# Kernel tuning notes

Hardware: AMD Instinct MI355X
Metric: run time of the kernel (lower is better)

Reference implementation:

```python
import jax, jax.numpy as jnp
import numpy as np

B, K, N, T, C = 2, 2, 4096, 8, 3
H = 192            # hidden_dim
NODE_DIM = 10
N_LAYERS = 10
KNN = 16           # k nearest neighbours
TOP_FRAC = 0.4
SHARP = 5.0        # mask_sharpness
S = max(int(TOP_FRAC * N), KNN + 1)   # n_select per graph


def _ln(x, g, b, eps=1e-5):
    mu = x.mean(-1, keepdims=True)
    v = ((x - mu) ** 2).mean(-1, keepdims=True)  # biased var, matches nn.LayerNorm
    return (x - mu) / jnp.sqrt(v + eps) * g + b


def setup_inputs() -> dict:
    key = jax.random.key(0)
    ks = jax.random.split(key, 12)
    rn = lambda k, shape: 0.05 * jax.random.normal(k, shape, jnp.float32)
    F0 = 2 * NODE_DIM + 4   # first EdgeConv MLP in-dim
    FR = 2 * H + 4          # remaining EdgeConv MLP in-dim
    L = N_LAYERS - 1
    return {
        "u_base": jax.random.normal(ks[0], (B, K, N, C), jnp.float32),
        "pos": jax.random.uniform(ks[1], (B, N, 3), dtype=jnp.float32),
        "velocity_in": jax.random.normal(ks[2], (B, T, N, C), jnp.float32),
        "airfoil_mask": (jax.random.uniform(ks[3], (B, N)) < 0.05).astype(jnp.float32),
        "conv0_w1": rn(ks[4], (F0, H)), "conv0_b1": jnp.zeros((H,)),
        "conv0_w2": rn(ks[5], (H, H)), "conv0_b2": jnp.zeros((H,)),
        "conv0_g": jnp.ones((H,)), "conv0_be": jnp.zeros((H,)),
        "convs_w1": rn(ks[6], (L, FR, H)), "convs_b1": jnp.zeros((L, H)),
        "convs_w2": rn(ks[7], (L, H, H)), "convs_b2": jnp.zeros((L, H)),
        "convs_g": jnp.ones((L, H)), "convs_be": jnp.zeros((L, H)),
        "head_g": jnp.ones((H,)), "head_be": jnp.zeros((H,)),
        "head_w1": rn(ks[8], (H, H)), "head_b1": jnp.zeros((H,)),
        "head_w2": rn(ks[9], (H, 3)), "head_b2": jnp.zeros((3,)),
    }


def reference(u_base, pos, velocity_in, airfoil_mask,
              conv0_w1, conv0_b1, conv0_w2, conv0_b2, conv0_g, conv0_be,
              convs_w1, convs_b1, convs_w2, convs_b2, convs_g, convs_be,
              head_g, head_be, head_w1, head_b1, head_w2, head_b2):
    # --- variance gating (torch .var/.std are unbiased) ---
    var_pp = jnp.var(velocity_in, axis=1, ddof=1).sum(-1)                      # [B,N]
    var_z = (var_pp - var_pp.mean(1, keepdims=True)) / (
        jnp.std(var_pp, axis=1, ddof=1, keepdims=True) + 1e-8)
    soft_mask = jax.nn.sigmoid(SHARP * var_z) * (1.0 - airfoil_mask)           # [B,N]

    # --- select top-variance points per graph ---
    _, top_idx = jax.lax.top_k(var_pp, S)                                      # [B,S]
    pos_sel = jnp.take_along_axis(pos, top_idx[..., None], axis=1)             # [B,S,3]
    mask_sel = jnp.take_along_axis(soft_mask, top_idx, axis=1)[..., None]      # [B,S,1]
    v_last = velocity_in[:, -1]                                                # [B,N,C]
    ub_sel = jnp.take_along_axis(u_base, top_idx[:, None, :, None], axis=2)    # [B,K,S,C]
    vl_sel = jnp.take_along_axis(v_last, top_idx[..., None], axis=1)           # [B,S,C]
    vf_sel = jnp.take_along_axis(var_pp[..., None], top_idx[..., None], axis=1)
    static = jnp.concatenate([vl_sel, pos_sel, vf_sel], -1)                    # [B,S,7]
    x0 = jnp.concatenate(
        [ub_sel, jnp.broadcast_to(static[:, None], (B, K, S, 7))], -1)         # [B,K,S,10]

    def per_graph(x, pos_b):  # x: [K,S,F0], pos_b: [S,3]
        # kNN graph (self excluded via +inf diagonal, as in the chunked cdist)
        d2 = jnp.sum((pos_b[:, None] - pos_b[None]) ** 2, -1)                  # [S,S]
        d2 = d2.at[jnp.arange(S), jnp.arange(S)].set(jnp.inf)
        _, knn = jax.lax.top_k(-d2, KNN)                                       # [S,KNN]
        # PyG convention with edge_index=stack([targets, sources]):
        # i = edge_index[1] = knn neighbours, j = edge_index[0] = centre nodes
        idx_i = knn.reshape(-1)                     # [E] aggregation targets
        idx_j = jnp.repeat(jnp.arange(S), KNN)      # [E]
        rel = pos_b[idx_i] - pos_b[idx_j]           # pos[edge_index[1]] - pos[edge_index[0]]
        dist = jnp.linalg.norm(rel, axis=-1, keepdims=True)
        ea = jnp.concatenate([rel, dist], -1)       # [E,4]
        ea_b = jnp.broadcast_to(ea, (K,) + ea.shape)

        def conv(h, w1, b1, w2, b2, g, be):
            hi = h[:, idx_i]
            hj = h[:, idx_j]
            m = jnp.concatenate([hi, hj - hi, ea_b], -1)                       # [K,E,2F+4]
            m = jax.nn.gelu(m @ w1 + b1, approximate=False) @ w2 + b2          # [K,E,H]
            agg = jnp.zeros((K, S, H), h.dtype).at[:, idx_i].add(m)
            return _ln(agg, g, be)

        h = conv(x, conv0_w1, conv0_b1, conv0_w2, conv0_b2, conv0_g, conv0_be)
        for l in range(N_LAYERS - 1):
            h = conv(h, convs_w1[l], convs_b1[l], convs_w2[l], convs_b2[l],
                     convs_g[l], convs_be[l]) + h
        hh = _ln(h, head_g, head_be)
        return jax.nn.gelu(hh @ head_w1 + head_b1, approximate=False) @ head_w2 + head_b2

    delta = jax.vmap(per_graph)(x0, pos_sel)        # [B,K,S,3]
    delta = delta * mask_sel[:, None]               # [B,1,S,1]

    def scatter_b(idx, d):  # idx [S], d [K,S,3]
        return jnp.zeros((K, N, C), d.dtype).at[:, idx].set(d)

    delta_full = jax.vmap(scatter_b)(top_idx, delta)            # [B,K,N,C]
    return (u_base + delta_full) * (1.0 - airfoil_mask)[:, None, :, None]
```

## Files before the change

### kernel.cpp

```cpp
#include <hip/hip_runtime.h>
#include <hip/hip_bf16.h>
#include <math.h>

#define B_ 2
#define K_ 2
#define NN_ 4096
#define T_ 8
#define C_ 3
#define H_ 192
#define S_ 1638
#define KK_ 16
#define E_ (S_*KK_)
#define NROW (B_*K_*S_)
#define SHARP_ 5.0f

typedef __hip_bfloat16 bf;
typedef unsigned long long ull;
typedef __bf16 bf16x8 __attribute__((ext_vector_type(8)));
typedef float f32x4 __attribute__((ext_vector_type(4)));

__device__ int   g_isbf16;
__device__ __align__(16) float g_var[B_*NN_];
__device__ __align__(16) float g_vs1[B_*16];
__device__ __align__(16) float g_vs2[B_*16];
__device__ __align__(16) int   g_topidx[B_*S_];
__device__ __align__(16) float g_possel[B_*S_*3];
__device__ __align__(16) float g_masksel[B_*S_];
__device__ __align__(16) float g_x0[NROW*10];
__device__ __align__(16) int   g_knn[B_*E_];
__device__ __align__(16) float g_ea[B_*E_*4];
__device__ __align__(16) int   g_indeg[B_*S_];
__device__ __align__(16) int   g_cursor[B_*S_];
__device__ __align__(16) int   g_off[B_*(S_+1)];
__device__ __align__(16) int   g_list[B_*E_];
__device__ __align__(16) float g_P[(size_t)NROW*H_];
__device__ __align__(16) bf    g_Qbf[(size_t)NROW*H_];
__device__ __align__(16) float g_h[(size_t)NROW*H_];
__device__ __align__(16) bf    g_w2p[(size_t)11*H_*H_];
__device__ __align__(16) bf    g_wcp[(size_t)9*H_*384];

__device__ __forceinline__ float bf2f(bf x){ return __bfloat162float(x); }
__device__ __forceinline__ float LD(const void* p, long i){
  return g_isbf16 ? __bfloat162float(((const bf*)p)[i]) : ((const float*)p)[i];
}
__device__ __forceinline__ float LDi(const void* p, long i, int isb){
  return isb ? __bfloat162float(((const bf*)p)[i]) : ((const float*)p)[i];
}
__device__ __forceinline__ float gelu_f(float x){ return 0.5f*x*(1.0f + erff(x*0.70710678118654752f)); }
__device__ __forceinline__ ull shfl_xor_u64(ull v, int m){
  unsigned lo = (unsigned)v, hi = (unsigned)(v >> 32);
  lo = __shfl_xor(lo, m, 64); hi = __shfl_xor(hi, m, 64);
  return ((ull)hi << 32) | lo;
}

__global__ __launch_bounds__(256) void k_var(const void* __restrict__ vel,
                                             const void* __restrict__ ub,
                                             const void* __restrict__ pos){
  __shared__ int s_bad;
  int b = blockIdx.y;
  int bx = blockIdx.x;
  int tid = threadIdx.x;
  if (tid == 0) s_bad = 0;
  __syncthreads();
  {
    const bf* pa = (const bf*)ub; const bf* pb = (const bf*)pos; const bf* pc = (const bf*)vel;
    int bad = 0;
    #pragma unroll
    for (int s = 0; s < 2; ++s){
      float va = __bfloat162float(pa[tid + s*256]);
      float vb = __bfloat162float(pb[tid + s*256]);
      float vc = __bfloat162float(pc[tid + s*256]);
      if (!(fabsf(va) <= 1000.f)) bad = 1;
      if (!(fabsf(vb) <= 1000.f)) bad = 1;
      if (!(fabsf(vc) <= 1000.f)) bad = 1;
    }
    if (bad) atomicOr(&s_bad, 1);
  }
  __syncthreads();
  int isb = (s_bad == 0) ? 1 : 0;
  if (bx == 0 && b == 0 && tid == 0) g_isbf16 = isb;
  int zi = (b*16 + bx)*256 + tid;
  if (zi < B_*S_){ g_indeg[zi] = 0; g_cursor[zi] = 0; }
  int n = bx*256 + tid;
  float v = 0.f;
  #pragma unroll
  for (int c = 0; c < 3; ++c){
    float x[8];
    #pragma unroll
    for (int t = 0; t < 8; ++t)
      x[t] = LDi(vel, ((long)(b*T_+t)*NN_ + n)*3 + c, isb);
    float m = __fadd_rn(__fadd_rn(__fadd_rn(x[0],x[1]), __fadd_rn(x[2],x[3])),
                        __fadd_rn(__fadd_rn(x[4],x[5]), __fadd_rn(x[6],x[7]))) / 8.0f;
    float d[8];
    #pragma unroll
    for (int t = 0; t < 8; ++t){ float dd = __fadd_rn(x[t], -m); d[t] = __fmul_rn(dd,dd); }
    float sv = __fadd_rn(__fadd_rn(__fadd_rn(d[0],d[1]), __fadd_rn(d[2],d[3])),
                         __fadd_rn(__fadd_rn(d[4],d[5]), __fadd_rn(d[6],d[7])));
    v = __fadd_rn(v, sv / 7.0f);
  }
  g_var[b*NN_ + n] = v;
  float s1 = v, s2 = v*v;
  #pragma unroll
  for (int o = 32; o; o >>= 1){ s1 += __shfl_xor(s1,o,64); s2 += __shfl_xor(s2,o,64); }
  __shared__ float r1[4], r2[4];
  int lane = tid & 63, wid = tid >> 6;
  if (!lane){ r1[wid]=s1; r2[wid]=s2; }
  __syncthreads();
  if (tid == 0){
    g_vs1[b*16 + bx] = r1[0]+r1[1]+r1[2]+r1[3];
    g_vs2[b*16 + bx] = r2[0]+r2[1]+r2[2]+r2[3];
  }
}

__global__ __launch_bounds__(256) void k_rank(){
  int b = blockIdx.y;
  int i = blockIdx.x*4 + (threadIdx.x >> 6);
  int lane = threadIdx.x & 63;
  float vi = g_var[b*NN_+i];
  int rank = 0;
  for (int j = lane; j < NN_; j += 64){
    float vj = g_var[b*NN_+j];
    rank += ((vj > vi) || (vj == vi && j < i)) ? 1 : 0;
  }
  #pragma unroll
  for (int o = 32; o; o >>= 1) rank += __shfl_xor(rank, o, 64);
  if (lane == 0 && rank < S_) g_topidx[b*S_ + rank] = i;
}

__global__ void k_gather(const void* __restrict__ pos, const void* __restrict__ ub,
                         const void* __restrict__ vel, const void* __restrict__ air){
  int gi = blockIdx.x*256 + threadIdx.x;
  if (gi >= B_*S_) return;
  int b = gi / S_, s = gi - b*S_;
  int node = g_topidx[gi];
  float px = LD(pos, ((long)b*NN_+node)*3+0);
  float py = LD(pos, ((long)b*NN_+node)*3+1);
  float pz = LD(pos, ((long)b*NN_+node)*3+2);
  g_possel[gi*3+0]=px; g_possel[gi*3+1]=py; g_possel[gi*3+2]=pz;
  float S1 = 0.f, S2 = 0.f;
  #pragma unroll
  for (int t = 0; t < 16; ++t){ S1 += g_vs1[b*16+t]; S2 += g_vs2[b*16+t]; }
  float mean = S1*(1.f/NN_);
  float sd = sqrtf(fmaxf((S2 - S1*S1*(1.f/NN_))*(1.f/(NN_-1)), 0.f));
  float vf = g_var[b*NN_+node];
  float z = (vf-mean)/(sd+1e-8f);
  float sig = 1.f/(1.f+expf(-SHARP_*z));
  g_masksel[gi] = sig*(1.f - LD(air, b*NN_+node));
  float vl0 = LD(vel, ((long)(b*T_+7)*NN_+node)*3+0);
  float vl1 = LD(vel, ((long)(b*T_+7)*NN_+node)*3+1);
  float vl2 = LD(vel, ((long)(b*T_+7)*NN_+node)*3+2);
  for (int k = 0; k < K_; ++k){
    long row = (long)(b*K_+k)*S_ + s;
    float* x = g_x0 + row*10;
    x[0]=LD(ub, ((long)(b*K_+k)*NN_+node)*3+0);
    x[1]=LD(ub, ((long)(b*K_+k)*NN_+node)*3+1);
    x[2]=LD(ub, ((long)(b*K_+k)*NN_+node)*3+2);
    x[3]=vl0; x[4]=vl1; x[5]=vl2;
    x[6]=px;  x[7]=py;  x[8]=pz;
    x[9]=vf;
  }
}

__global__ __launch_bounds__(256) void k_knn(){
  __shared__ float px[S_], py[S_], pz[S_];
  int b = blockIdx.y;
  int j = blockIdx.x*4 + (threadIdx.x >> 6);
  int lane = threadIdx.x & 63;
  for (int t = threadIdx.x; t < S_; t += 256){
    px[t] = g_possel[(b*S_+t)*3+0];
    py[t] = g_possel[(b*S_+t)*3+1];
    pz[t] = g_possel[(b*S_+t)*3+2];
  }
  __syncthreads();
  if (j >= S_) return;
  float xj=px[j], yj=py[j], zj=pz[j];
  float dist[KK_]; int id[KK_];
  #pragma unroll
  for (int t = 0; t < KK_; ++t){ dist[t]=3.0e38f; id[t]=0x7fffffff; }
  for (int c = lane; c < S_; c += 64){
    if (c == j) continue;
    float dx=__fadd_rn(px[c],-xj), dy=__fadd_rn(py[c],-yj), dz=__fadd_rn(pz[c],-zj);
    float d2 = __fadd_rn(__fadd_rn(__fmul_rn(dx,dx), __fmul_rn(dy,dy)), __fmul_rn(dz,dz));
    if (d2 < dist[KK_-1]){
      int p = 0;
      #pragma unroll
      for (int q = 0; q < KK_; ++q) p += (dist[q] <= d2) ? 1 : 0;
      #pragma unroll
      for (int q = KK_-1; q >= 1; --q){
        bool mv = (q > p);
        dist[q] = mv ? dist[q-1] : dist[q];
        id[q]   = mv ? id[q-1]   : id[q];
      }
      #pragma unroll
      for (int q = 0; q < KK_; ++q){ if (q == p){ dist[q] = d2; id[q] = c; } }
    }
  }
  ull mykey = 0;
  #pragma unroll
  for (int t = 0; t < KK_; ++t){
    ull k = (((ull)__float_as_uint(dist[0])) << 32) | (unsigned)id[0];
    ull m = k;
    #pragma unroll
    for (int o = 32; o; o >>= 1){ ull other = shfl_xor_u64(m, o); m = (other < m) ? other : m; }
    if (k == m){
      #pragma unroll
      for (int q = 0; q < KK_-1; ++q){ dist[q]=dist[q+1]; id[q]=id[q+1]; }
      dist[KK_-1] = 3.0e38f; id[KK_-1] = 0x7fffffff;
    }
    if (lane == t) mykey = m;
  }
  if (lane < KK_){
    int i = (int)(mykey & 0xffffffffu);
    g_knn[(b*S_+j)*KK_ + lane] = i;
    float rx = __fadd_rn(px[i],-xj), ry = __fadd_rn(py[i],-yj), rz = __fadd_rn(pz[i],-zj);
    float dd = sqrtf(__fadd_rn(__fadd_rn(__fmul_rn(rx,rx), __fmul_rn(ry,ry)), __fmul_rn(rz,rz)));
    float* o = g_ea + ((long)b*E_ + j*KK_ + lane)*4;
    o[0]=rx; o[1]=ry; o[2]=rz; o[3]=dd;
    atomicAdd(&g_indeg[b*S_+i], 1);
  }
}

__global__ void k_scan(){
  __shared__ int sA[2048], sB[2048];
  int b = blockIdx.x, tid = threadIdx.x;
  for (int i = tid; i < 2048; i += 1024) sA[i] = (i < S_) ? g_indeg[b*S_+i] : 0;
  __syncthreads();
  int *src = sA, *dst = sB;
  for (int d = 1; d < 2048; d <<= 1){
    for (int i = tid; i < 2048; i += 1024) dst[i] = src[i] + (i >= d ? src[i-d] : 0);
    __syncthreads();
    int* t2 = src; src = dst; dst = t2;
  }
  if (tid == 0) g_off[b*(S_+1)] = 0;
  for (int i = tid; i < S_; i += 1024) g_off[b*(S_+1)+i+1] = src[i];
}

#define PW2_BLKS 1584
#define PWC_BLKS 2592
#define INIT_BLKS 192
#define FILL_BLKS 205
#define PROJ_BLKS 410
__global__ void k_packall(const void* __restrict__ c0w2, const void* __restrict__ cw2,
                          const void* __restrict__ hw1, const void* __restrict__ cw1,
                          const void* __restrict__ ub, const void* __restrict__ air,
                          float* __restrict__ out, const void* __restrict__ c0w1){
  int blk = blockIdx.x;
  if (blk < PW2_BLKS){
    int gi = blk*256 + threadIdx.x;
    if (gi >= 11*H_*H_) return;
    int mat = gi / (H_*H_), r = gi - mat*(H_*H_);
    int k = r / H_, n = r - (r/H_)*H_;
    float v;
    if (mat == 0)      v = LD(c0w2, (long)k*H_ + n);
    else if (mat <= 9) v = LD(cw2, (long)(mat-1)*H_*H_ + (long)k*H_ + n);
    else               v = LD(hw1, (long)k*H_ + n);
    int t = k>>5, q = (k>>3)&3, jj = k&7;
    g_w2p[(size_t)mat*H_*H_ + (((t*4+q)*H_ + n)*8 + jj)] = __float2bfloat16(v);
  } else if (blk < PW2_BLKS + PWC_BLKS){
    int gi = (blk - PW2_BLKS)*256 + threadIdx.x;
    if (gi >= 9*H_*384) return;
    int l = gi / (H_*384), r = gi - l*(H_*384);
    int k = r / 384, n = r - (r/384)*384;
    long base = (long)l*388*H_;
    float v;
    if (n < H_) v = LD(cw1, base + (long)k*H_ + n) - LD(cw1, base + (long)(H_+k)*H_ + n);
    else        v = LD(cw1, base + (long)(H_+k)*H_ + (n-H_));
    int t = k>>5, q = (k>>3)&3, jj = k&7;
    g_wcp[(size_t)l*(H_*384) + (((t*4+q)*384 + n)*8 + jj)] = __float2bfloat16(v);
  } else if (blk < PW2_BLKS + PWC_BLKS + INIT_BLKS){
    int gi = (blk - PW2_BLKS - PWC_BLKS)*256 + threadIdx.x;
    int n = (gi/3) % NN_;
    int b = gi / (K_*NN_*C_);
    float a = 1.f - LD(air, b*NN_+n);
    out[gi] = LD(ub, gi) * a;
  } else if (blk < PW2_BLKS + PWC_BLKS + INIT_BLKS + FILL_BLKS){
    int idx = (blk - PW2_BLKS - PWC_BLKS - INIT_BLKS)*256 + threadIdx.x;
    if (idx >= B_*E_) return;
    int b = idx / E_, e = idx - b*E_;
    int i = g_knn[idx];
    int slot = atomicAdd(&g_cursor[b*S_+i], 1);
    g_list[b*E_ + g_off[b*(S_+1)+i] + slot] = e;
  } else {
    __shared__ float xs[16][10];
    __shared__ float wP[10][192];
    __shared__ float wQ[10][192];
    int tid = threadIdx.x;
    long rowBase = (long)(blk - PW2_BLKS - PWC_BLKS - INIT_BLKS - FILL_BLKS) * 16;
    for (int idx = tid; idx < 1920; idx += 256){
      int f = idx / 192, n = idx - (idx/192)*192;
      float a = LD(c0w1, f*H_+n), b = LD(c0w1, (10+f)*H_+n);
      wP[f][n] = a - b; wQ[f][n] = b;
    }
    for (int idx = tid; idx < 160; idx += 256){
      int r = idx / 10, f = idx - (idx/10)*10;
      long row = rowBase + r; if (row >= NROW) row = NROW-1;
      xs[r][f] = g_x0[row*10 + f];
    }
    __syncthreads();
    for (int o = tid; o < 16*384; o += 256){
      int r = o / 384, n = o - (o/384)*384;
      long row = rowBase + r;
      if (row >= NROW) continue;
      float acc = 0.f;
      if (n < 192){
        #pragma unroll
        for (int f = 0; f < 10; ++f) acc += xs[r][f]*wP[f][n];
        g_P[row*192 + n] = acc;
      } else {
        int nc = n - 192;
        #pragma unroll
        for (int f = 0; f < 10; ++f) acc += xs[r][f]*wQ[f][nc];
        g_Qbf[row*192 + nc] = __float2bfloat16(acc);
      }
    }
  }
}

template<int RES, int DOPQ, int DOHEAD>
__global__ __launch_bounds__(256) void k_layer(
    const void* __restrict__ w1cB, long w1cO,
    const void* __restrict__ b1B, long b1O,
    const void* __restrict__ biasB, long biasO,
    const void* __restrict__ gB, long gO,
    const void* __restrict__ beB, long beO,
    int bOff, int pqOff,
    const void* __restrict__ hg, const void* __restrict__ hbe,
    const void* __restrict__ hb1, const void* __restrict__ hw2,
    const void* __restrict__ hb2, const void* __restrict__ ubase,
    const void* __restrict__ air, float* __restrict__ out,
    int M){
  int wv = threadIdx.x >> 6, lane = threadIdx.x & 63;
  int q = lane >> 4, l16 = lane & 15;
  long rowBase = (long)blockIdx.x * 8;
  __shared__ bf    sbf[16][200];
  __shared__ float tile[8][200];
  __shared__ float ws0[192], ws1[192], ws2[192], ws3[192], b1s[192], gs[192], bes[192];
  __shared__ float srow[8], rrow[8];
  for (int c = threadIdx.x; c < 192; c += 256){
    ws0[c] = LD(w1cB, w1cO+c);
    ws1[c] = LD(w1cB, w1cO+H_+c);
    ws2[c] = LD(w1cB, w1cO+2*H_+c);
    ws3[c] = LD(w1cB, w1cO+3*H_+c);
    b1s[c] = LD(b1B, b1O+c);
    gs[c]  = LD(gB, gO+c);
    bes[c] = LD(beB, beO+c);
  }
  for (int o = threadIdx.x; o < 8*192; o += 256){
    int lr = o / 192, col = o - lr*192;
    sbf[8+lr][col] = __float2bfloat16(0.f);
  }
  __syncthreads();
  for (int rr = 0; rr < 2; ++rr){
    int lrow = wv*2 + rr;
    long row = rowBase + lrow;
    int bk = (int)(row / S_); int i = (int)(row - (long)bk*S_); int b = bk >> 1;
    int off = __builtin_amdgcn_readfirstlane(g_off[b*(S_+1)+i]);
    int deg = __builtin_amdgcn_readfirstlane(g_off[b*(S_+1)+i+1]) - off;
    const int* lst = g_list + b*E_ + off;
    const bf* Q = g_Qbf + (size_t)bk*S_*H_;
    const float* EA = g_ea + (size_t)b*E_*4;
    int c0 = lane, c1 = lane+64, c2 = lane+128;
    float w00=ws0[c0], w01=ws1[c0], w02=ws2[c0], w03=ws3[c0];
    float w10=ws0[c1], w11=ws1[c1], w12=ws2[c1], w13=ws3[c1];
    float w20=ws0[c2], w21=ws1[c2], w22=ws2[c2], w23=ws3[c2];
    float base0 = g_P[(size_t)row*H_+c0] + b1s[c0];
    float base1 = g_P[(size_t)row*H_+c1] + b1s[c1];
    float base2 = g_P[(size_t)row*H_+c2] + b1s[c2];
    float acc0=0.f, acc1=0.f, acc2=0.f;
    int d = 0;
    for (; d + 2 <= deg; d += 2){
      int e0 = __builtin_amdgcn_readfirstlane(lst[d]);
      int e1 = __builtin_amdgcn_readfirstlane(lst[d+1]);
      float4 a0 = *reinterpret_cast<const float4*>(EA + (size_t)e0*4);
      float4 a1 = *reinterpret_cast<const float4*>(EA + (size_t)e1*4);
      const bf* Q0 = Q + (size_t)(e0>>4)*H_;
      const bf* Q1 = Q + (size_t)(e1>>4)*H_;
      float q00=bf2f(Q0[c0]), q01=bf2f(Q0[c1]), q02=bf2f(Q0[c2]);
      float q10=bf2f(Q1[c0]), q11=bf2f(Q1[c1]), q12=bf2f(Q1[c2]);
      float g00 = gelu_f(base0 + q00 + a0.x*w00 + a0.y*w01 + a0.z*w02 + a0.w*w03);
      float g01 = gelu_f(base1 + q01 + a0.x*w10 + a0.y*w11 + a0.z*w12 + a0.w*w13);
      float g02 = gelu_f(base2 + q02 + a0.x*w20 + a0.y*w21 + a0.z*w22 + a0.w*w23);
      float g10 = gelu_f(base0 + q10 + a1.x*w00 + a1.y*w01 + a1.z*w02 + a1.w*w03);
      float g11 = gelu_f(base1 + q11 + a1.x*w10 + a1.y*w11 + a1.z*w12 + a1.w*w13);
      float g12 = gelu_f(base2 + q12 + a1.x*w20 + a1.y*w21 + a1.z*w22 + a1.w*w23);
      acc0 += g00; acc0 += g10;
      acc1 += g01; acc1 += g11;
      acc2 += g02; acc2 += g12;
    }
    for (; d < deg; ++d){
      int e = __builtin_amdgcn_readfirstlane(lst[d]);
      float4 a = *reinterpret_cast<const float4*>(EA + (size_t)e*4);
      const bf* Qe = Q + (size_t)(e>>4)*H_;
      acc0 += gelu_f(base0 + bf2f(Qe[c0]) + a.x*w00 + a.y*w01 + a.z*w02 + a.w*w03);
      acc1 += gelu_f(base1 + bf2f(Qe[c1]) + a.x*w10 + a.y*w11 + a.z*w12 + a.w*w13);
      acc2 += gelu_f(base2 + bf2f(Qe[c2]) + a.x*w20 + a.y*w21 + a.z*w22 + a.w*w23);
    }
    sbf[lrow][c0] = __float2bfloat16(acc0);
    sbf[lrow][c1] = __float2bfloat16(acc1);
    sbf[lrow][c2] = __float2bfloat16(acc2);
  }
  __syncthreads();
  {
    const bf* Bp = g_w2p + bOff;
    f32x4 acc[3];
    #pragma unroll
    for (int ct = 0; ct < 3; ++ct) acc[ct] = (f32x4){0.f,0.f,0.f,0.f};
    #pragma unroll
    for (int t = 0; t < 6; ++t){
      int kof = t*32 + q*8;
      bf16x8 af = *reinterpret_cast<const bf16x8*>(&sbf[l16][kof]);
      #pragma unroll
      for (int ct = 0; ct < 3; ++ct){
        int n = wv*48 + ct*16 + l16;
        bf16x8 bfr = *reinterpret_cast<const bf16x8*>(Bp + (((t*4+q)*192 + n)*8));
        acc[ct] = __builtin_amdgcn_mfma_f32_16x16x32_bf16(af, bfr, acc[ct], 0,0,0);
      }
    }
    float degf[4];
    #pragma unroll
    for (int r = 0; r < 4; ++r){
      int lr = q*4 + r;
      if (lr < 8){
        long row = rowBase + lr;
        int bk = (int)(row / S_); int i = (int)(row - (long)bk*S_); int b = bk >> 1;
        degf[r] = (float)(g_off[b*(S_+1)+i+1] - g_off[b*(S_+1)+i]);
      } else degf[r] = 0.f;
    }
    #pragma unroll
    for (int ct = 0; ct < 3; ++ct){
      int col = wv*48 + ct*16 + l16;
      float bb = LD(biasB, biasO + col);
      #pragma unroll
      for (int r = 0; r < 4; ++r){
        int lr = q*4 + r;
        if (lr < 8) tile[lr][col] = acc[ct][r] + degf[r]*bb;
      }
    }
  }
  __syncthreads();
  {
    int lr = threadIdx.x >> 5;
    int k32 = threadIdx.x & 31;
    float s = 0.f, qq = 0.f;
    #pragma unroll
    for (int c6 = 0; c6 < 6; ++c6){ float x = tile[lr][k32 + c6*32]; s += x; qq += x*x; }
    #pragma unroll
    for (int o = 1; o < 32; o <<= 1){ s += __shfl_xor(s,o,64); qq += __shfl_xor(qq,o,64); }
    if (k32 == 0){
      float mu = s*(1.f/H_);
      float var = qq*(1.f/H_) - mu*mu;
      srow[lr] = mu;
      rrow[lr] = rsqrtf(fmaxf(var, 0.f) + 1e-5f);
    }
  }
  __syncthreads();
  for (int o = threadIdx.x; o < 8*192; o += 256){
    int lr = o / 192, col = o - lr*192;
    long row = rowBase + lr;
    float y = (tile[lr][col] - srow[lr])*rrow[lr]*gs[col] + bes[col];
    if (RES) y += g_h[(size_t)row*192 + col];
    if (!DOHEAD) g_h[(size_t)row*192 + col] = y;
    sbf[lr][col] = __float2bfloat16(y);
    if (DOHEAD) tile[lr][col] = y;
  }
  if (DOPQ){
    __syncthreads();
    const bf* Bq = g_wcp + pqOff;
    f32x4 acc2[6];
    #pragma unroll
    for (int ct = 0; ct < 6; ++ct) acc2[ct] = (f32x4){0.f,0.f,0.f,0.f};
    #pragma unroll
    for (int t = 0; t < 6; ++t){
      int kof = t*32 + q*8;
      bf16x8 af = *reinterpret_cast<const bf16x8*>(&sbf[l16][kof]);
      #pragma unroll
      for (int ct = 0; ct < 6; ++ct){
        int n = wv*96 + ct*16 + l16;
        bf16x8 bfr = *reinterpret_cast<const bf16x8*>(Bq + (((t*4+q)*384 + n)*8));
        acc2[ct] = __builtin_amdgcn_mfma_f32_16x16x32_bf16(af, bfr, acc2[ct], 0,0,0);
      }
    }
    #pragma unroll
    for (int ct = 0; ct < 6; ++ct){
      int col = wv*96 + ct*16 + l16;
      #pragma unroll
      for (int r = 0; r < 4; ++r){
        int orow = q*4 + r;
        if (orow < 8){
          long row = rowBase + orow;
          float v = acc2[ct][r];
          if (col < 192) g_P[(size_t)row*192 + col] = v;
          else           g_Qbf[(size_t)row*192 + (col-192)] = __float2bfloat16(v);
        }
      }
    }
  }
  if (DOHEAD){
    __syncthreads();
    {
      int lr = threadIdx.x >> 5;
      int k32 = threadIdx.x & 31;
      float s = 0.f, qq = 0.f;
      #pragma unroll
      for (int c6 = 0; c6 < 6; ++c6){ float x = tile[lr][k32 + c6*32]; s += x; qq += x*x; }
      #pragma unroll
      for (int o = 1; o < 32; o <<= 1){ s += __shfl_xor(s,o,64); qq += __shfl_xor(qq,o,64); }
      if (k32 == 0){
        float mu = s*(1.f/H_);
        float var = qq*(1.f/H_) - mu*mu;
        srow[lr] = mu;
        rrow[lr] = rsqrtf(fmaxf(var, 0.f) + 1e-5f);
      }
    }
    __syncthreads();
    for (int o = threadIdx.x; o < 8*192; o += 256){
      int lr = o / 192, col = o - lr*192;
      sbf[lr][col] = __float2bfloat16((tile[lr][col] - srow[lr])*rrow[lr]*LD(hg,col) + LD(hbe,col));
    }
    __syncthreads();
    {
      const bf* Bp = g_w2p + 10*H_*H_;
      f32x4 hacc[3];
      #pragma unroll
      for (int ct = 0; ct < 3; ++ct) hacc[ct] = (f32x4){0.f,0.f,0.f,0.f};
      #pragma unroll
      for (int t = 0; t < 6; ++t){
        int kof = t*32 + q*8;
        bf16x8 af = *reinterpret_cast<const bf16x8*>(&sbf[l16][kof]);
        #pragma unroll
        for (int ct = 0; ct < 3; ++ct){
          int n = wv*48 + ct*16 + l16;
          bf16x8 bfr = *reinterpret_cast<const bf16x8*>(Bp + (((t*4+q)*192 + n)*8));
          hacc[ct] = __builtin_amdgcn_mfma_f32_16x16x32_bf16(af, bfr, hacc[ct], 0,0,0);
        }
      }
      #pragma unroll
      for (int ct = 0; ct < 3; ++ct){
        int col = wv*48 + ct*16 + l16;
        float bb = LD(hb1, col);
        #pragma unroll
        for (int r = 0; r < 4; ++r){
          int lr = q*4 + r;
          if (lr < 8) tile[lr][col] = gelu_f(hacc[ct][r] + bb);
        }
      }
    }
    __syncthreads();
    {
      int r = threadIdx.x >> 5, k32 = threadIdx.x & 31;
      float p0 = 0.f, p1 = 0.f, p2 = 0.f;
      #pragma unroll
      for (int c6 = 0; c6 < 6; ++c6){
        int col = k32 + c6*32;
        float tv = tile[r][col];
        p0 += tv*LD(hw2, col*3+0);
        p1 += tv*LD(hw2, col*3+1);
        p2 += tv*LD(hw2, col*3+2);
      }
      #pragma unroll
      for (int o = 1; o < 32; o <<= 1){
        p0 += __shfl_xor(p0,o,64);
        p1 += __shfl_xor(p1,o,64);
        p2 += __shfl_xor(p2,o,64);
      }
      if (k32 == 0){
        long row = rowBase + r;
        int bk = (int)(row / S_), s = (int)(row - (long)bk*S_), b = bk >> 1;
        float msk = g_masksel[b*S_+s];
        int node = g_topidx[b*S_+s];
        float am = 1.f - LD(air, b*NN_+node);
        float d0 = p0 + LD(hb2,0), d1 = p1 + LD(hb2,1), d2 = p2 + LD(hb2,2);
        long oi = ((long)bk*NN_ + node)*3;
        out[oi+0] = (LD(ubase, oi+0) + d0*msk)*am;
        out[oi+1] = (LD(ubase, oi+1) + d1*msk)*am;
        out[oi+2] = (LD(ubase, oi+2) + d2*msk)*am;
      }
    }
  }
}

extern "C" void kernel_launch(void* const* d_in, const int* in_sizes, int n_in,
                              void* d_out, int out_size, void* d_ws, size_t ws_size,
                              hipStream_t stream) {
  (void)in_sizes; (void)n_in; (void)d_ws; (void)ws_size; (void)out_size;
  const void* u_base = d_in[0];
  const void* pos    = d_in[1];
  const void* vel    = d_in[2];
  const void* air    = d_in[3];
  const void* c0w1   = d_in[4];
  const void* c0b1   = d_in[5];
  const void* c0w2   = d_in[6];
  const void* c0b2   = d_in[7];
  const void* c0g    = d_in[8];
  const void* c0be   = d_in[9];
  const void* cw1    = d_in[10];
  const void* cb1    = d_in[11];
  const void* cw2    = d_in[12];
  const void* cb2    = d_in[13];
  const void* cg     = d_in[14];
  const void* cbe    = d_in[15];
  const void* hg     = d_in[16];
  const void* hbe    = d_in[17];
  const void* hw1    = d_in[18];
  const void* hb1    = d_in[19];
  const void* hw2    = d_in[20];
  const void* hb2    = d_in[21];
  float* out = (float*)d_out;

  k_var<<<dim3(16, B_), 256, 0, stream>>>(vel, u_base, pos);
  k_rank<<<dim3(NN_/4, B_), 256, 0, stream>>>();
  k_gather<<<13, 256, 0, stream>>>(pos, u_base, vel, air);
  k_knn<<<dim3((S_+3)/4, B_), 256, 0, stream>>>();
  k_scan<<<B_, 1024, 0, stream>>>();
  k_packall<<<PW2_BLKS + PWC_BLKS + INIT_BLKS + FILL_BLKS + PROJ_BLKS, 256, 0, stream>>>(
      c0w2, cw2, hw1, cw1, u_base, air, out, c0w1);

  const int GN8 = NROW / 8;
  for (int l = 0; l < 10; ++l){
    long w1cO = (l == 0) ? 20L*H_ : ((long)(l-1)*388 + 384)*H_;
    const void* w1cB = (l == 0) ? c0w1 : cw1;
    long lOff = (l == 0) ? 0 : (long)(l-1)*H_;
    const void* b1B = (l == 0) ? c0b1 : cb1;
    const void* b2B = (l == 0) ? c0b2 : cb2;
    const void* gB  = (l == 0) ? c0g  : cg;
    const void* beB = (l == 0) ? c0be : cbe;
    if (l == 0)
      k_layer<0,1,0><<<GN8, 256, 0, stream>>>(w1cB, w1cO, b1B, lOff, b2B, lOff, gB, lOff, beB, lOff,
                                              0, 0, hg, hbe, hb1, hw2, hb2, u_base, air, out, NROW);
    else if (l < 9)
      k_layer<1,1,0><<<GN8, 256, 0, stream>>>(w1cB, w1cO, b1B, lOff, b2B, lOff, gB, lOff, beB, lOff,
                                              l*H_*H_, l*H_*384, hg, hbe, hb1, hw2, hb2, u_base, air, out, NROW);
    else
      k_layer<1,0,1><<<GN8, 256, 0, stream>>>(w1cB, w1cO, b1B, lOff, b2B, lOff, gB, lOff, beB, lOff,
                                              l*H_*H_, 0, hg, hbe, hb1, hw2, hb2, u_base, air, out, NROW);
  }
}
```

Measured before the change: 667.0 us.

## Use 512-thread layer blocks with one row per wave and ping-pong Q buffers

The per-layer kernel now runs with 512 threads, so each of the 8 waves handles one destination row instead of two. The MFMA column tiles, the LayerNorm reductions and the head reductions are remapped to match. The edge gather loop is unrolled by 4 instead of 2, exposing more independent loads and GELU evaluations per wave. The Q projection is double-buffered by layer parity, so a layer no longer overwrites Q values that other blocks may still be reading. This adds extra global memory and leaves some waves idle in the 192-column GEMM, since only 12 tiles are spread over 8 waves.

```diff
diff --git a/kernel.cpp b/kernel.cpp
--- a/kernel.cpp
+++ b/kernel.cpp
@@ -34,7 +34,7 @@
 __device__ __align__(16) int   g_off[B_*(S_+1)];
 __device__ __align__(16) int   g_list[B_*E_];
 __device__ __align__(16) float g_P[(size_t)NROW*H_];
-__device__ __align__(16) bf    g_Qbf[(size_t)NROW*H_];
+__device__ __align__(16) bf    g_Qbf[2*(size_t)NROW*H_];
 __device__ __align__(16) float g_h[(size_t)NROW*H_];
 __device__ __align__(16) bf    g_w2p[(size_t)11*H_*H_];
 __device__ __align__(16) bf    g_wcp[(size_t)9*H_*384];
@@ -317,26 +317,27 @@
 }
 
 template<int RES, int DOPQ, int DOHEAD>
-__global__ __launch_bounds__(256) void k_layer(
+__global__ __launch_bounds__(512) void k_layer(
     const void* __restrict__ w1cB, long w1cO,
     const void* __restrict__ b1B, long b1O,
     const void* __restrict__ biasB, long biasO,
     const void* __restrict__ gB, long gO,
     const void* __restrict__ beB, long beO,
-    int bOff, int pqOff,
+    int bOff, int pqOff, int qcur, int qnxt,
     const void* __restrict__ hg, const void* __restrict__ hbe,
     const void* __restrict__ hb1, const void* __restrict__ hw2,
     const void* __restrict__ hb2, const void* __restrict__ ubase,
     const void* __restrict__ air, float* __restrict__ out,
     int M){
-  int wv = threadIdx.x >> 6, lane = threadIdx.x & 63;
+  int tid = threadIdx.x;
+  int wv = tid >> 6, lane = tid & 63;
   int q = lane >> 4, l16 = lane & 15;
   long rowBase = (long)blockIdx.x * 8;
   __shared__ bf    sbf[16][200];
   __shared__ float tile[8][200];
   __shared__ float ws0[192], ws1[192], ws2[192], ws3[192], b1s[192], gs[192], bes[192];
   __shared__ float srow[8], rrow[8];
-  for (int c = threadIdx.x; c < 192; c += 256){
+  for (int c = tid; c < 192; c += 512){
     ws0[c] = LD(w1cB, w1cO+c);
     ws1[c] = LD(w1cB, w1cO+H_+c);
     ws2[c] = LD(w1cB, w1cO+2*H_+c);
@@ -345,19 +346,18 @@
     gs[c]  = LD(gB, gO+c);
     bes[c] = LD(beB, beO+c);
   }
-  for (int o = threadIdx.x; o < 8*192; o += 256){
+  for (int o = tid; o < 8*192; o += 512){
     int lr = o / 192, col = o - lr*192;
     sbf[8+lr][col] = __float2bfloat16(0.f);
   }
   __syncthreads();
-  for (int rr = 0; rr < 2; ++rr){
-    int lrow = wv*2 + rr;
-    long row = rowBase + lrow;
+  {
+    long row = rowBase + wv;
     int bk = (int)(row / S_); int i = (int)(row - (long)bk*S_); int b = bk >> 1;
-    int off = __builtin_amdgcn_readfirstlane(g_off[b*(S_+1)+i]);
-    int deg = __builtin_amdgcn_readfirstlane(g_off[b*(S_+1)+i+1]) - off;
+    int off = g_off[b*(S_+1)+i];
+    int deg = g_off[b*(S_+1)+i+1] - off;
     const int* lst = g_list + b*E_ + off;
-    const bf* Q = g_Qbf + (size_t)bk*S_*H_;
+    const bf* Q = g_Qbf + (size_t)qcur*NROW*H_ + (size_t)bk*S_*H_;
     const float* EA = g_ea + (size_t)b*E_*4;
     int c0 = lane, c1 = lane+64, c2 = lane+128;
     float w00=ws0[c0], w01=ws1[c0], w02=ws2[c0], w03=ws3[c0];
@@ -368,52 +368,63 @@
     float base2 = g_P[(size_t)row*H_+c2] + b1s[c2];
     float acc0=0.f, acc1=0.f, acc2=0.f;
     int d = 0;
-    for (; d + 2 <= deg; d += 2){
-      int e0 = __builtin_amdgcn_readfirstlane(lst[d]);
-      int e1 = __builtin_amdgcn_readfirstlane(lst[d+1]);
+    for (; d + 4 <= deg; d += 4){
+      int e0 = lst[d], e1 = lst[d+1], e2 = lst[d+2], e3 = lst[d+3];
       float4 a0 = *reinterpret_cast<const float4*>(EA + (size_t)e0*4);
       float4 a1 = *reinterpret_cast<const float4*>(EA + (size_t)e1*4);
+      float4 a2 = *reinterpret_cast<const float4*>(EA + (size_t)e2*4);
+      float4 a3 = *reinterpret_cast<const float4*>(EA + (size_t)e3*4);
       const bf* Q0 = Q + (size_t)(e0>>4)*H_;
       const bf* Q1 = Q + (size_t)(e1>>4)*H_;
+      const bf* Q2 = Q + (size_t)(e2>>4)*H_;
+      const bf* Q3 = Q + (size_t)(e3>>4)*H_;
       float q00=bf2f(Q0[c0]), q01=bf2f(Q0[c1]), q02=bf2f(Q0[c2]);
       float q10=bf2f(Q1[c0]), q11=bf2f(Q1[c1]), q12=bf2f(Q1[c2]);
-      float g00 = gelu_f(base0 + q00 + a0.x*w00 + a0.y*w01 + a0.z*w02 + a0.w*w03);
-      float g01 = gelu_f(base1 + q01 + a0.x*w10 + a0.y*w11 + a0.z*w12 + a0.w*w13);
-      float g02 = gelu_f(base2 + q02 + a0.x*w20 + a0.y*w21 + a0.z*w22 + a0.w*w23);
-      float g10 = gelu_f(base0 + q10 + a1.x*w00 + a1.y*w01 + a1.z*w02 + a1.w*w03);
-      float g11 = gelu_f(base1 + q11 + a1.x*w10 + a1.y*w11 + a1.z*w12 + a1.w*w13);
-      float g12 = gelu_f(base2 + q12 + a1.x*w20 + a1.y*w21 + a1.z*w22 + a1.w*w23);
-      acc0 += g00; acc0 += g10;
-      acc1 += g01; acc1 += g11;
-      acc2 += g02; acc2 += g12;
+      float q20=bf2f(Q2[c0]), q21=bf2f(Q2[c1]), q22=bf2f(Q2[c2]);
+      float q30=bf2f(Q3[c0]), q31=bf2f(Q3[c1]), q32=bf2f(Q3[c2]);
+      acc0 += gelu_f(base0 + q00 + a0.x*w00 + a0.y*w01 + a0.z*w02 + a0.w*w03);
+      acc0 += gelu_f(base0 + q10 + a1.x*w00 + a1.y*w01 + a1.z*w02 + a1.w*w03);
+      acc0 += gelu_f(base0 + q20 + a2.x*w00 + a2.y*w01 + a2.z*w02 + a2.w*w03);
+      acc0 += gelu_f(base0 + q30 + a3.x*w00 + a3.y*w01 + a3.z*w02 + a3.w*w03);
+      acc1 += gelu_f(base1 + q01 + a0.x*w10 + a0.y*w11 + a0.z*w12 + a0.w*w13);
+      acc1 += gelu_f(base1 + q11 + a1.x*w10 + a1.y*w11 + a1.z*w12 + a1.w*w13);
+      acc1 += gelu_f(base1 + q21 + a2.x*w10 + a2.y*w11 + a2.z*w12 + a2.w*w13);
+      acc1 += gelu_f(base1 + q31 + a3.x*w10 + a3.y*w11 + a3.z*w12 + a3.w*w13);
+      acc2 += gelu_f(base2 + q02 + a0.x*w20 + a0.y*w21 + a0.z*w22 + a0.w*w23);
+      acc2 += gelu_f(base2 + q12 + a1.x*w20 + a1.y*w21 + a1.z*w22 + a1.w*w23);
+      acc2 += gelu_f(base2 + q22 + a2.x*w20 + a2.y*w21 + a2.z*w22 + a2.w*w23);
+      acc2 += gelu_f(base2 + q32 + a3.x*w20 + a3.y*w21 + a3.z*w22 + a3.w*w23);
     }
     for (; d < deg; ++d){
-      int e = __builtin_amdgcn_readfirstlane(lst[d]);
+      int e = lst[d];
       float4 a = *reinterpret_cast<const float4*>(EA + (size_t)e*4);
       const bf* Qe = Q + (size_t)(e>>4)*H_;
       acc0 += gelu_f(base0 + bf2f(Qe[c0]) + a.x*w00 + a.y*w01 + a.z*w02 + a.w*w03);
       acc1 += gelu_f(base1 + bf2f(Qe[c1]) + a.x*w10 + a.y*w11 + a.z*w12 + a.w*w13);
       acc2 += gelu_f(base2 + bf2f(Qe[c2]) + a.x*w20 + a.y*w21 + a.z*w22 + a.w*w23);
     }
-    sbf[lrow][c0] = __float2bfloat16(acc0);
-    sbf[lrow][c1] = __float2bfloat16(acc1);
-    sbf[lrow][c2] = __float2bfloat16(acc2);
+    sbf[wv][c0] = __float2bfloat16(acc0);
+    sbf[wv][c1] = __float2bfloat16(acc1);
+    sbf[wv][c2] = __float2bfloat16(acc2);
   }
   __syncthreads();
   {
     const bf* Bp = g_w2p + bOff;
-    f32x4 acc[3];
-    #pragma unroll
-    for (int ct = 0; ct < 3; ++ct) acc[ct] = (f32x4){0.f,0.f,0.f,0.f};
+    f32x4 acc[2];
+    acc[0] = (f32x4){0.f,0.f,0.f,0.f};
+    acc[1] = (f32x4){0.f,0.f,0.f,0.f};
     #pragma unroll
     for (int t = 0; t < 6; ++t){
       int kof = t*32 + q*8;
       bf16x8 af = *reinterpret_cast<const bf16x8*>(&sbf[l16][kof]);
       #pragma unroll
-      for (int ct = 0; ct < 3; ++ct){
-        int n = wv*48 + ct*16 + l16;
-        bf16x8 bfr = *reinterpret_cast<const bf16x8*>(Bp + (((t*4+q)*192 + n)*8));
-        acc[ct] = __builtin_amdgcn_mfma_f32_16x16x32_bf16(af, bfr, acc[ct], 0,0,0);
+      for (int jj = 0; jj < 2; ++jj){
+        int j = wv + jj*8;
+        if (j < 12){
+          int n = j*16 + l16;
+          bf16x8 bfr = *reinterpret_cast<const bf16x8*>(Bp + (((t*4+q)*192 + n)*8));
+          acc[jj] = __builtin_amdgcn_mfma_f32_16x16x32_bf16(af, bfr, acc[jj], 0,0,0);
+        }
       }
     }
     float degf[4];
@@ -427,34 +438,35 @@
       } else degf[r] = 0.f;
     }
     #pragma unroll
-    for (int ct = 0; ct < 3; ++ct){
-      int col = wv*48 + ct*16 + l16;
-      float bb = LD(biasB, biasO + col);
-      #pragma unroll
-      for (int r = 0; r < 4; ++r){
-        int lr = q*4 + r;
-        if (lr < 8) tile[lr][col] = acc[ct][r] + degf[r]*bb;
+    for (int jj = 0; jj < 2; ++jj){
+      int j = wv + jj*8;
+      if (j < 12){
+        int col = j*16 + l16;
+        float bb = LD(biasB, biasO + col);
+        #pragma unroll
+        for (int r = 0; r < 4; ++r){
+          int lr = q*4 + r;
+          if (lr < 8) tile[lr][col] = acc[jj][r] + degf[r]*bb;
+        }
       }
     }
   }
   __syncthreads();
   {
-    int lr = threadIdx.x >> 5;
-    int k32 = threadIdx.x & 31;
     float s = 0.f, qq = 0.f;
     #pragma unroll
-    for (int c6 = 0; c6 < 6; ++c6){ float x = tile[lr][k32 + c6*32]; s += x; qq += x*x; }
-    #pragma unroll
-    for (int o = 1; o < 32; o <<= 1){ s += __shfl_xor(s,o,64); qq += __shfl_xor(qq,o,64); }
-    if (k32 == 0){
+    for (int c3 = 0; c3 < 3; ++c3){ float x = tile[wv][lane + c3*64]; s += x; qq += x*x; }
+    #pragma unroll
+    for (int o = 1; o < 64; o <<= 1){ s += __shfl_xor(s,o,64); qq += __shfl_xor(qq,o,64); }
+    if (lane == 0){
       float mu = s*(1.f/H_);
       float var = qq*(1.f/H_) - mu*mu;
-      srow[lr] = mu;
-      rrow[lr] = rsqrtf(fmaxf(var, 0.f) + 1e-5f);
-    }
-  }
-  __syncthreads();
-  for (int o = threadIdx.x; o < 8*192; o += 256){
+      srow[wv] = mu;
+      rrow[wv] = rsqrtf(fmaxf(var, 0.f) + 1e-5f);
+    }
+  }
+  __syncthreads();
+  for (int o = tid; o < 8*192; o += 512){
     int lr = o / 192, col = o - lr*192;
     long row = rowBase + lr;
     float y = (tile[lr][col] - srow[lr])*rrow[lr]*gs[col] + bes[col];
@@ -466,31 +478,32 @@
   if (DOPQ){
     __syncthreads();
     const bf* Bq = g_wcp + pqOff;
-    f32x4 acc2[6];
-    #pragma unroll
-    for (int ct = 0; ct < 6; ++ct) acc2[ct] = (f32x4){0.f,0.f,0.f,0.f};
+    bf* Qout = g_Qbf + (size_t)qnxt*NROW*H_;
+    f32x4 acc2[3];
+    #pragma unroll
+    for (int jj = 0; jj < 3; ++jj) acc2[jj] = (f32x4){0.f,0.f,0.f,0.f};
     #pragma unroll
     for (int t = 0; t < 6; ++t){
       int kof = t*32 + q*8;
       bf16x8 af = *reinterpret_cast<const bf16x8*>(&sbf[l16][kof]);
       #pragma unroll
-      for (int ct = 0; ct < 6; ++ct){
-        int n = wv*96 + ct*16 + l16;
+      for (int jj = 0; jj < 3; ++jj){
+        int n = (wv*3 + jj)*16 + l16;
         bf16x8 bfr = *reinterpret_cast<const bf16x8*>(Bq + (((t*4+q)*384 + n)*8));
-        acc2[ct] = __builtin_amdgcn_mfma_f32_16x16x32_bf16(af, bfr, acc2[ct], 0,0,0);
-      }
-    }
-    #pragma unroll
-    for (int ct = 0; ct < 6; ++ct){
-      int col = wv*96 + ct*16 + l16;
+        acc2[jj] = __builtin_amdgcn_mfma_f32_16x16x32_bf16(af, bfr, acc2[jj], 0,0,0);
+      }
+    }
+    #pragma unroll
+    for (int jj = 0; jj < 3; ++jj){
+      int col = (wv*3 + jj)*16 + l16;
       #pragma unroll
       for (int r = 0; r < 4; ++r){
         int orow = q*4 + r;
         if (orow < 8){
           long row = rowBase + orow;
-          float v = acc2[ct][r];
+          float v = acc2[jj][r];
           if (col < 192) g_P[(size_t)row*192 + col] = v;
-          else           g_Qbf[(size_t)row*192 + (col-192)] = __float2bfloat16(v);
+          else           Qout[(size_t)row*192 + (col-192)] = __float2bfloat16(v);
         }
       }
     }
@@ -498,73 +511,77 @@
   if (DOHEAD){
     __syncthreads();
     {
-      int lr = threadIdx.x >> 5;
-      int k32 = threadIdx.x & 31;
       float s = 0.f, qq = 0.f;
       #pragma unroll
-      for (int c6 = 0; c6 < 6; ++c6){ float x = tile[lr][k32 + c6*32]; s += x; qq += x*x; }
-      #pragma unroll
-      for (int o = 1; o < 32; o <<= 1){ s += __shfl_xor(s,o,64); qq += __shfl_xor(qq,o,64); }
-      if (k32 == 0){
+      for (int c3 = 0; c3 < 3; ++c3){ float x = tile[wv][lane + c3*64]; s += x; qq += x*x; }
+      #pragma unroll
+      for (int o = 1; o < 64; o <<= 1){ s += __shfl_xor(s,o,64); qq += __shfl_xor(qq,o,64); }
+      if (lane == 0){
         float mu = s*(1.f/H_);
         float var = qq*(1.f/H_) - mu*mu;
-        srow[lr] = mu;
-        rrow[lr] = rsqrtf(fmaxf(var, 0.f) + 1e-5f);
+        srow[wv] = mu;
+        rrow[wv] = rsqrtf(fmaxf(var, 0.f) + 1e-5f);
       }
     }
     __syncthreads();
-    for (int o = threadIdx.x; o < 8*192; o += 256){
+    for (int o = tid; o < 8*192; o += 512){
       int lr = o / 192, col = o - lr*192;
       sbf[lr][col] = __float2bfloat16((tile[lr][col] - srow[lr])*rrow[lr]*LD(hg,col) + LD(hbe,col));
     }
     __syncthreads();
     {
       const bf* Bp = g_w2p + 10*H_*H_;
-      f32x4 hacc[3];
-      #pragma unroll
-      for (int ct = 0; ct < 3; ++ct) hacc[ct] = (f32x4){0.f,0.f,0.f,0.f};
+      f32x4 hacc[2];
+      hacc[0] = (f32x4){0.f,0.f,0.f,0.f};
+      hacc[1] = (f32x4){0.f,0.f,0.f,0.f};
       #pragma unroll
       for (int t = 0; t < 6; ++t){
         int kof = t*32 + q*8;
         bf16x8 af = *reinterpret_cast<const bf16x8*>(&sbf[l16][kof]);
         #pragma unroll
-        for (int ct = 0; ct < 3; ++ct){
-          int n = wv*48 + ct*16 + l16;
-          bf16x8 bfr = *reinterpret_cast<const bf16x8*>(Bp + (((t*4+q)*192 + n)*8));
-          hacc[ct] = __builtin_amdgcn_mfma_f32_16x16x32_bf16(af, bfr, hacc[ct], 0,0,0);
+        for (int jj = 0; jj < 2; ++jj){
+          int j = wv + jj*8;
+          if (j < 12){
+            int n = j*16 + l16;
+            bf16x8 bfr = *reinterpret_cast<const bf16x8*>(Bp + (((t*4+q)*192 + n)*8));
+            hacc[jj] = __builtin_amdgcn_mfma_f32_16x16x32_bf16(af, bfr, hacc[jj], 0,0,0);
+          }
         }
       }
-      #pragma unroll
-      for (int ct = 0; ct < 3; ++ct){
-        int col = wv*48 + ct*16 + l16;
-        float bb = LD(hb1, col);
-        #pragma unroll
-        for (int r = 0; r < 4; ++r){
-          int lr = q*4 + r;
-          if (lr < 8) tile[lr][col] = gelu_f(hacc[ct][r] + bb);
+      __syncthreads();
+      #pragma unroll
+      for (int jj = 0; jj < 2; ++jj){
+        int j = wv + jj*8;
+        if (j < 12){
+          int col = j*16 + l16;
+          float bb = LD(hb1, col);
+          #pragma unroll
+          for (int r = 0; r < 4; ++r){
+            int lr = q*4 + r;
+            if (lr < 8) tile[lr][col] = gelu_f(hacc[jj][r] + bb);
+          }
         }
       }
     }
     __syncthreads();
     {
-      int r = threadIdx.x >> 5, k32 = threadIdx.x & 31;
       float p0 = 0.f, p1 = 0.f, p2 = 0.f;
       #pragma unroll
-      for (int c6 = 0; c6 < 6; ++c6){
-        int col = k32 + c6*32;
-        float tv = tile[r][col];
+      for (int c3 = 0; c3 < 3; ++c3){
+        int col = lane + c3*64;
+        float tv = tile[wv][col];
         p0 += tv*LD(hw2, col*3+0);
         p1 += tv*LD(hw2, col*3+1);
         p2 += tv*LD(hw2, col*3+2);
       }
       #pragma unroll
-      for (int o = 1; o < 32; o <<= 1){
+      for (int o = 1; o < 64; o <<= 1){
         p0 += __shfl_xor(p0,o,64);
         p1 += __shfl_xor(p1,o,64);
         p2 += __shfl_xor(p2,o,64);
       }
-      if (k32 == 0){
-        long row = rowBase + r;
+      if (lane == 0){
+        long row = rowBase + wv;
         int bk = (int)(row / S_), s = (int)(row - (long)bk*S_), b = bk >> 1;
         float msk = g_masksel[b*S_+s];
         int node = g_topidx[b*S_+s];
@@ -624,14 +641,15 @@
     const void* b2B = (l == 0) ? c0b2 : cb2;
     const void* gB  = (l == 0) ? c0g  : cg;
     const void* beB = (l == 0) ? c0be : cbe;
+    int qcur = l & 1, qnxt = (l+1) & 1;
     if (l == 0)
-      k_layer<0,1,0><<<GN8, 256, 0, stream>>>(w1cB, w1cO, b1B, lOff, b2B, lOff, gB, lOff, beB, lOff,
-                                              0, 0, hg, hbe, hb1, hw2, hb2, u_base, air, out, NROW);
+      k_layer<0,1,0><<<GN8, 512, 0, stream>>>(w1cB, w1cO, b1B, lOff, b2B, lOff, gB, lOff, beB, lOff,
+                                              0, 0, qcur, qnxt, hg, hbe, hb1, hw2, hb2, u_base, air, out, NROW);
     else if (l < 9)
-      k_layer<1,1,0><<<GN8, 256, 0, stream>>>(w1cB, w1cO, b1B, lOff, b2B, lOff, gB, lOff, beB, lOff,
-                                              l*H_*H_, l*H_*384, hg, hbe, hb1, hw2, hb2, u_base, air, out, NROW);
+      k_layer<1,1,0><<<GN8, 512, 0, stream>>>(w1cB, w1cO, b1B, lOff, b2B, lOff, gB, lOff, beB, lOff,
+                                              l*H_*H_, l*H_*384, qcur, qnxt, hg, hbe, hb1, hw2, hb2, u_base, air, out, NROW);
     else
-      k_layer<1,0,1><<<GN8, 256, 0, stream>>>(w1cB, w1cO, b1B, lOff, b2B, lOff, gB, lOff, beB, lOff,
-                                              l*H_*H_, 0, hg, hbe, hb1, hw2, hb2, u_base, air, out, NROW);
-  }
-}
+      k_layer<1,0,1><<<GN8, 512, 0, stream>>>(w1cB, w1cO, b1B, lOff, b2B, lOff, gB, lOff, beB, lOff,
+                                              l*H_*H_, 0, qcur, qnxt, hg, hbe, hb1, hw2, hb2, u_base, air, out, NROW);
+  }
+}
```

New measurement: 695.7 us. 4.3% more time.
